# Performance work log

Hardware: AMD Instinct MI355X
Metric: run time of the kernel (lower is better)

The kernel has to match this reference:

```python
import jax, jax.numpy as jnp
import numpy as np

B, S, D = 2, 2048, 2048
H = 16
HD = D // H  # 128


def setup_inputs() -> dict:
    key = jax.random.key(0)
    ks = jax.random.split(key, 9)
    s = 1.0 / np.sqrt(D)
    return {
        "hidden_states": jax.random.normal(ks[0], (B, S, D), dtype=jnp.float32),
        "Wq": jax.random.normal(ks[1], (D, D), dtype=jnp.float32) * s,
        "bq": jnp.zeros((D,), dtype=jnp.float32),
        "Wk": jax.random.normal(ks[2], (D, D), dtype=jnp.float32) * s,
        "bk": jnp.zeros((D,), dtype=jnp.float32),
        "Wv": jax.random.normal(ks[3], (D, D), dtype=jnp.float32) * s,
        "bv": jnp.zeros((D,), dtype=jnp.float32),
        "Wo": jax.random.normal(ks[4], (D, D), dtype=jnp.float32) * s,
        "bo": jnp.zeros((D,), dtype=jnp.float32),
    }


def reference(hidden_states, Wq, bq, Wk, bk, Wv, bv, Wo, bo):
    x = hidden_states
    # linear projections (torch Linear: x @ W.T + b)
    q = x @ Wq.T + bq
    k = x @ Wk.T + bk
    v = x @ Wv.T + bv
    # [B, S, H, HD] -> [B, H, S, HD]
    q = q.reshape(B, S, H, HD).transpose(0, 2, 1, 3)
    k = k.reshape(B, S, H, HD).transpose(0, 2, 1, 3)
    v = v.reshape(B, S, H, HD).transpose(0, 2, 1, 3)
    q = q / jnp.sqrt(jnp.float32(HD))
    # scores [B, H, S, S]
    scores = jnp.einsum("bhqd,bhkd->bhqk", q, k)
    causal = jnp.triu(jnp.full((S, S), -jnp.inf, dtype=scores.dtype), k=1)
    scores = scores + causal
    attn = jax.nn.softmax(scores, axis=-1)
    out = jnp.einsum("bhqk,bhkd->bhqd", attn, v)
    out = out.transpose(0, 2, 1, 3).reshape(B, S, D)
    return out @ Wo.T + bo
```

## Files before the change

### kernel.cpp

```cpp
#include <hip/hip_runtime.h>
#include <stdint.h>

#define S_LEN 2048
#define DMODEL 2048
#define NHEAD 16
#define HDIM 128

typedef __attribute__((ext_vector_type(8))) short short8;
typedef __attribute__((ext_vector_type(4))) float floatx4;

__device__ __forceinline__ unsigned short f2b(float f) {
  union { float f; unsigned u; } v; v.f = f;
  unsigned r = v.u + 0x7FFFu + ((v.u >> 16) & 1u);
  return (unsigned short)(r >> 16);
}

__device__ __forceinline__ void load_lds16(const unsigned short* g, unsigned short* l) {
  __builtin_amdgcn_global_load_lds((const __attribute__((address_space(1))) void*)g,
                                   (__attribute__((address_space(3))) void*)l, 16, 0, 0);
}

__global__ __launch_bounds__(256) void cvt_all(const float* __restrict__ x,
                                               const float* __restrict__ Wq, const float* __restrict__ Wk,
                                               const float* __restrict__ Wv, const float* __restrict__ Wo,
                                               unsigned short* __restrict__ xb,
                                               unsigned short* __restrict__ Wqb, unsigned short* __restrict__ Wkb,
                                               unsigned short* __restrict__ Wvb, unsigned short* __restrict__ Wob) {
  const size_t idx = (size_t)blockIdx.x * 256 + threadIdx.x;
  const int y = blockIdx.y;
  const float4* s; ushort4* d;
  if (y == 0)      { s = (const float4*)x;               d = (ushort4*)xb; }
  else if (y == 1) { s = (const float4*)x + (1u << 20);  d = (ushort4*)xb + (1u << 20); }
  else if (y == 2) { s = (const float4*)Wq;              d = (ushort4*)Wqb; }
  else if (y == 3) { s = (const float4*)Wk;              d = (ushort4*)Wkb; }
  else if (y == 4) { s = (const float4*)Wv;              d = (ushort4*)Wvb; }
  else             { s = (const float4*)Wo;              d = (ushort4*)Wob; }
  float4 f = s[idx];
  ushort4 o;
  o.x = f2b(f.x); o.y = f2b(f.y); o.z = f2b(f.z); o.w = f2b(f.w);
  d[idx] = o;
}

template <int MODE>
__global__ __launch_bounds__(256)
void gemm_bt(const unsigned short* __restrict__ A, const unsigned short* __restrict__ Bw,
             const float* __restrict__ bias, void* __restrict__ Cout,
             int M, int N, int K, float scale) {
  __shared__ unsigned short As[128 * 64];
  __shared__ unsigned short Bs[128 * 64];
  const int t = threadIdx.x;
  const int lane = t & 63, wave = t >> 6;
  const int quad = lane >> 4, lc = lane & 15;
  const int wm = wave >> 1, wn = wave & 1;
  const int m0 = blockIdx.y * 128, n0 = blockIdx.x * 128;

  const int srow = lane >> 3;
  const int skoff = ((lane & 7) ^ srow) * 8;
  const unsigned short* Ag[4];
  const unsigned short* Bg[4];
  unsigned short* Al[4];
  unsigned short* Bl[4];
#pragma unroll
  for (int i = 0; i < 4; i++) {
    int c = wave * 4 + i;
    Ag[i] = A + (size_t)(m0 + c * 8 + srow) * K + skoff;
    Bg[i] = Bw + (size_t)(n0 + c * 8 + srow) * K + skoff;
    Al[i] = &As[c * 512 + lane * 8];
    Bl[i] = &Bs[c * 512 + lane * 8];
  }

  int koff[2];
#pragma unroll
  for (int ks = 0; ks < 2; ks++) koff[ks] = ((ks * 4 + quad) ^ (lc & 7)) * 8;

  floatx4 acc[4][4] = {};

  for (int kt = 0; kt < K; kt += 64) {
    if (kt) __syncthreads();
#pragma unroll
    for (int i = 0; i < 4; i++) {
      load_lds16(Ag[i] + kt, Al[i]);
      load_lds16(Bg[i] + kt, Bl[i]);
    }
    __syncthreads();
#pragma unroll
    for (int ks = 0; ks < 2; ks++) {
      short8 av[4], bv[4];
#pragma unroll
      for (int mt = 0; mt < 4; mt++)
        av[mt] = *(const short8*)&As[(wm * 64 + mt * 16 + lc) * 64 + koff[ks]];
#pragma unroll
      for (int nt = 0; nt < 4; nt++)
        bv[nt] = *(const short8*)&Bs[(wn * 64 + nt * 16 + lc) * 64 + koff[ks]];
#pragma unroll
      for (int mt = 0; mt < 4; mt++)
#pragma unroll
        for (int nt = 0; nt < 4; nt++)
          acc[mt][nt] = __builtin_amdgcn_mfma_f32_16x16x32_bf16(av[mt], bv[nt], acc[mt][nt], 0, 0, 0);
    }
  }

#pragma unroll
  for (int nt = 0; nt < 4; nt++) {
    const int col = n0 + wn * 64 + nt * 16 + lc;
    const float bcol = bias[col];
#pragma unroll
    for (int mt = 0; mt < 4; mt++) {
      const int row0 = m0 + wm * 64 + mt * 16 + quad * 4;
      if (MODE == 1) {
        ushort4 o;
        o.x = f2b((acc[mt][nt][0] + bcol) * scale);
        o.y = f2b((acc[mt][nt][1] + bcol) * scale);
        o.z = f2b((acc[mt][nt][2] + bcol) * scale);
        o.w = f2b((acc[mt][nt][3] + bcol) * scale);
        int b = row0 >> 11;
        int s = row0 & (S_LEN - 1);
        *(ushort4*)&((unsigned short*)Cout)[((size_t)(b * DMODEL + col)) * S_LEN + s] = o;
      } else {
#pragma unroll
        for (int r = 0; r < 4; r++) {
          float v = (acc[mt][nt][r] + bcol) * scale;
          if (MODE == 2)
            ((float*)Cout)[(size_t)(row0 + r) * N + col] = v;
          else
            ((unsigned short*)Cout)[(size_t)(row0 + r) * N + col] = f2b(v);
        }
      }
    }
  }
}

__global__ __launch_bounds__(256, 2)
void attn_fwd(const unsigned short* __restrict__ Qg, const unsigned short* __restrict__ Kg,
              const unsigned short* __restrict__ Vtg, unsigned short* __restrict__ Og) {
  __shared__ unsigned short Ks[2][64 * 128];
  __shared__ unsigned short Vs[128 * 64];
  __shared__ unsigned short Ps[128 * 64];

  const int t = threadIdx.x;
  const int lane = t & 63, w = t >> 6;
  const int quad = lane >> 4, lc = lane & 15;
  const int y = blockIdx.y;
  const int tile = (y < 16) ? (int)blockIdx.x : 15 - (int)blockIdx.x;
  const int b = y >> 4, h = y & 15;
  const size_t qkbase = (size_t)b * S_LEN * DMODEL + h * HDIM;
  const size_t vtbase = ((size_t)(b * DMODEL + h * HDIM)) * S_LEN;
  const int q0 = tile * 128;
  const int wrow = q0 + w * 32;

  short8 aq[2][4];
#pragma unroll
  for (int pm = 0; pm < 2; pm++)
#pragma unroll
    for (int ks = 0; ks < 4; ks++)
      aq[pm][ks] = *(const short8*)&Qg[qkbase + (size_t)(wrow + pm * 16 + lc) * DMODEL + ks * 32 + quad * 8];

  const unsigned short* kga[4];
  const unsigned short* vga[4];
  int kloff[4], vloff[4];
#pragma unroll
  for (int i = 0; i < 4; i++) {
    int c = w * 4 + i;
    int krow = 4 * c + (lane >> 4);
    kga[i] = Kg + qkbase + (size_t)krow * DMODEL + ((lane & 15) ^ (krow & 15)) * 8;
    kloff[i] = c * 512 + lane * 8;
    int vrow = 8 * c + (lane >> 3);
    vga[i] = Vtg + vtbase + (size_t)vrow * S_LEN + ((lane & 7) ^ (vrow & 7)) * 8;
    vloff[i] = c * 512 + lane * 8;
  }

  floatx4 oacc[2][8] = {};
  float m_run[2][4], l_run[2][4];
#pragma unroll
  for (int pm = 0; pm < 2; pm++)
#pragma unroll
    for (int r = 0; r < 4; r++) { m_run[pm][r] = -1e30f; l_run[pm][r] = 0.f; }

  const int kiters = 2 * tile + 2;

#pragma unroll
  for (int i = 0; i < 4; i++) load_lds16(kga[i], &Ks[0][kloff[i]]);

  for (int kb = 0; kb < kiters; kb++) {
    const int k0 = kb * 64;
    const int cur = kb & 1;
    __syncthreads();

#pragma unroll
    for (int i = 0; i < 4; i++) load_lds16(vga[i] + k0, &Vs[vloff[i]]);
    {
      const size_t knext = (size_t)((kb + 1 < kiters) ? k0 + 64 : k0) * DMODEL;
#pragma unroll
      for (int i = 0; i < 4; i++) load_lds16(kga[i] + knext, &Ks[cur ^ 1][kloff[i]]);
    }

    const bool hasw = (k0 <= wrow + 31);
    floatx4 sacc[2][4];
    float alpha[2][4];
    if (hasw) {
#pragma unroll
      for (int pm = 0; pm < 2; pm++)
#pragma unroll
        for (int nt = 0; nt < 4; nt++) sacc[pm][nt] = (floatx4){0.f, 0.f, 0.f, 0.f};
#pragma unroll
      for (int ks = 0; ks < 4; ks++) {
        short8 bk[4];
#pragma unroll
        for (int nt = 0; nt < 4; nt++) {
          int n = nt * 16 + lc;
          bk[nt] = *(const short8*)&Ks[cur][n * 128 + (((ks * 4 + quad) ^ (n & 15)) * 8)];
        }
#pragma unroll
        for (int pm = 0; pm < 2; pm++)
#pragma unroll
          for (int nt = 0; nt < 4; nt++)
            sacc[pm][nt] = __builtin_amdgcn_mfma_f32_16x16x32_bf16(aq[pm][ks], bk[nt], sacc[pm][nt], 0, 0, 0);
      }

      float mx[2][4];
#pragma unroll
      for (int pm = 0; pm < 2; pm++)
#pragma unroll
        for (int r = 0; r < 4; r++) mx[pm][r] = -1e30f;
      if (k0 + 63 > wrow) {
#pragma unroll
        for (int pm = 0; pm < 2; pm++)
#pragma unroll
          for (int nt = 0; nt < 4; nt++) {
            int col = k0 + nt * 16 + lc;
#pragma unroll
            for (int r = 0; r < 4; r++) {
              if (col > wrow + pm * 16 + quad * 4 + r) sacc[pm][nt][r] = -1e30f;
              mx[pm][r] = fmaxf(mx[pm][r], sacc[pm][nt][r]);
            }
          }
      } else {
#pragma unroll
        for (int pm = 0; pm < 2; pm++)
#pragma unroll
          for (int nt = 0; nt < 4; nt++)
#pragma unroll
            for (int r = 0; r < 4; r++) mx[pm][r] = fmaxf(mx[pm][r], sacc[pm][nt][r]);
      }
#pragma unroll
      for (int off = 1; off < 16; off <<= 1)
#pragma unroll
        for (int pm = 0; pm < 2; pm++)
#pragma unroll
          for (int r = 0; r < 4; r++) mx[pm][r] = fmaxf(mx[pm][r], __shfl_xor(mx[pm][r], off));

#pragma unroll
      for (int pm = 0; pm < 2; pm++)
#pragma unroll
        for (int r = 0; r < 4; r++) {
          float mnew = fmaxf(m_run[pm][r], mx[pm][r]);
          alpha[pm][r] = __builtin_amdgcn_exp2f(m_run[pm][r] - mnew);
          m_run[pm][r] = mnew;
          l_run[pm][r] *= alpha[pm][r];
        }
#pragma unroll
      for (int pm = 0; pm < 2; pm++)
#pragma unroll
        for (int nt = 0; nt < 4; nt++) {
#pragma unroll
          for (int r = 0; r < 4; r++) {
            float p = __builtin_amdgcn_exp2f(sacc[pm][nt][r] - m_run[pm][r]);
            l_run[pm][r] += p;
            int row = w * 32 + pm * 16 + quad * 4 + r;
            int sw = (((nt * 2 + (lc >> 3)) ^ (row & 7)) * 8) + (lc & 7);
            Ps[row * 64 + sw] = f2b(p);
          }
        }
    }

    asm volatile("s_waitcnt vmcnt(4)\n\ts_barrier" ::: "memory");

    if (hasw) {
#pragma unroll
      for (int pm = 0; pm < 2; pm++)
#pragma unroll
        for (int nt8 = 0; nt8 < 8; nt8++)
#pragma unroll
          for (int r = 0; r < 4; r++) oacc[pm][nt8][r] *= alpha[pm][r];

#pragma unroll
      for (int ks = 0; ks < 2; ks++) {
        short8 ap[2];
#pragma unroll
        for (int pm = 0; pm < 2; pm++) {
          int m = w * 32 + pm * 16 + lc;
          ap[pm] = *(const short8*)&Ps[m * 64 + (((ks * 4 + quad) ^ (m & 7)) * 8)];
        }
#pragma unroll
        for (int nt8 = 0; nt8 < 8; nt8++) {
          int n = nt8 * 16 + lc;
          short8 bv = *(const short8*)&Vs[n * 64 + (((ks * 4 + quad) ^ (n & 7)) * 8)];
#pragma unroll
          for (int pm = 0; pm < 2; pm++)
            oacc[pm][nt8] = __builtin_amdgcn_mfma_f32_16x16x32_bf16(ap[pm], bv, oacc[pm][nt8], 0, 0, 0);
        }
      }
    }
  }

#pragma unroll
  for (int off = 1; off < 16; off <<= 1)
#pragma unroll
    for (int pm = 0; pm < 2; pm++)
#pragma unroll
      for (int r = 0; r < 4; r++) l_run[pm][r] += __shfl_xor(l_run[pm][r], off);
#pragma unroll
  for (int pm = 0; pm < 2; pm++)
#pragma unroll
    for (int r = 0; r < 4; r++) {
      float inv = 1.f / l_run[pm][r];
      size_t obase = ((size_t)(b * S_LEN + wrow + pm * 16 + quad * 4 + r)) * DMODEL + h * HDIM;
#pragma unroll
      for (int nt8 = 0; nt8 < 8; nt8++)
        Og[obase + nt8 * 16 + lc] = f2b(oacc[pm][nt8][r] * inv);
    }
}

extern "C" void kernel_launch(void* const* d_in, const int* in_sizes, int n_in,
                              void* d_out, int out_size, void* d_ws, size_t ws_size,
                              hipStream_t stream) {
  const float* x  = (const float*)d_in[0];
  const float* Wq = (const float*)d_in[1];
  const float* bq = (const float*)d_in[2];
  const float* Wk = (const float*)d_in[3];
  const float* bk = (const float*)d_in[4];
  const float* Wv = (const float*)d_in[5];
  const float* bv = (const float*)d_in[6];
  const float* Wo = (const float*)d_in[7];
  const float* bo = (const float*)d_in[8];

  const int M = 2 * S_LEN;
  const int N = DMODEL, K = DMODEL;

  char* w = (char*)d_ws;
  unsigned short* xb  = (unsigned short*)(w);
  unsigned short* Wqb = (unsigned short*)(w + (size_t)16 * (1 << 20));
  unsigned short* Wkb = (unsigned short*)(w + (size_t)24 * (1 << 20));
  unsigned short* Wvb = (unsigned short*)(w + (size_t)32 * (1 << 20));
  unsigned short* Wob = (unsigned short*)(w + (size_t)40 * (1 << 20));
  unsigned short* Qb  = (unsigned short*)(w + (size_t)48 * (1 << 20));
  unsigned short* Kb  = (unsigned short*)(w + (size_t)64 * (1 << 20));
  unsigned short* Vtb = (unsigned short*)(w + (size_t)80 * (1 << 20));
  unsigned short* Ob  = (unsigned short*)(w + (size_t)96 * (1 << 20));

  cvt_all<<<dim3(4096, 6), 256, 0, stream>>>(x, Wq, Wk, Wv, Wo, xb, Wqb, Wkb, Wvb, Wob);

  dim3 gg(N / 128, M / 128);
  const float qscale = 0.08838834764831843f * 1.4426950408889634f;
  gemm_bt<0><<<gg, 256, 0, stream>>>(xb, Wqb, bq, Qb, M, N, K, qscale);
  gemm_bt<0><<<gg, 256, 0, stream>>>(xb, Wkb, bk, Kb, M, N, K, 1.f);
  gemm_bt<1><<<gg, 256, 0, stream>>>(xb, Wvb, bv, Vtb, M, N, K, 1.f);

  attn_fwd<<<dim3(16, 32), 256, 0, stream>>>(Qb, Kb, Vtb, Ob);

  gemm_bt<2><<<gg, 256, 0, stream>>>(Ob, Wob, bo, d_out, M, N, K, 1.f);
}
```

Measured before the change: 396.5 us.

## Compute transposed S and O tiles so each lane owns a query row

Swaps MFMA operand order so score and output accumulators are transposed, with each lane holding one query row. The row max and row sum then need only two cross-lane shuffles instead of four per element group, and running max/sum state shrinks to two scalars per lane. P is written to LDS as packed 4-element vectors in a padded (stride 72) layout instead of scalar swizzled stores, and output is stored as ushort4. The padded P buffer uses slightly more LDS.

```diff
diff --git a/kernel.cpp b/kernel.cpp
--- a/kernel.cpp
+++ b/kernel.cpp
@@ -135,7 +135,7 @@
               const unsigned short* __restrict__ Vtg, unsigned short* __restrict__ Og) {
   __shared__ unsigned short Ks[2][64 * 128];
   __shared__ unsigned short Vs[128 * 64];
-  __shared__ unsigned short Ps[128 * 64];
+  __shared__ unsigned short Ps[128 * 72];
 
   const int t = threadIdx.x;
   const int lane = t & 63, w = t >> 6;
@@ -169,12 +169,8 @@
     vloff[i] = c * 512 + lane * 8;
   }
 
-  floatx4 oacc[2][8] = {};
-  float m_run[2][4], l_run[2][4];
-#pragma unroll
-  for (int pm = 0; pm < 2; pm++)
-#pragma unroll
-    for (int r = 0; r < 4; r++) { m_run[pm][r] = -1e30f; l_run[pm][r] = 0.f; }
+  floatx4 oaccT[8][2] = {};
+  float m_run[2] = {-1e30f, -1e30f}, l_run[2] = {0.f, 0.f};
 
   const int kiters = 2 * tile + 2;
 
@@ -195,130 +191,121 @@
     }
 
     const bool hasw = (k0 <= wrow + 31);
-    floatx4 sacc[2][4];
-    float alpha[2][4];
+    float alpha[2];
     if (hasw) {
-#pragma unroll
-      for (int pm = 0; pm < 2; pm++)
-#pragma unroll
-        for (int nt = 0; nt < 4; nt++) sacc[pm][nt] = (floatx4){0.f, 0.f, 0.f, 0.f};
+      floatx4 st[4][2];
+#pragma unroll
+      for (int mt = 0; mt < 4; mt++)
+#pragma unroll
+        for (int pm = 0; pm < 2; pm++) st[mt][pm] = (floatx4){0.f, 0.f, 0.f, 0.f};
 #pragma unroll
       for (int ks = 0; ks < 4; ks++) {
-        short8 bk[4];
-#pragma unroll
-        for (int nt = 0; nt < 4; nt++) {
-          int n = nt * 16 + lc;
-          bk[nt] = *(const short8*)&Ks[cur][n * 128 + (((ks * 4 + quad) ^ (n & 15)) * 8)];
-        }
-#pragma unroll
-        for (int pm = 0; pm < 2; pm++)
-#pragma unroll
-          for (int nt = 0; nt < 4; nt++)
-            sacc[pm][nt] = __builtin_amdgcn_mfma_f32_16x16x32_bf16(aq[pm][ks], bk[nt], sacc[pm][nt], 0, 0, 0);
-      }
-
-      float mx[2][4];
-#pragma unroll
-      for (int pm = 0; pm < 2; pm++)
-#pragma unroll
-        for (int r = 0; r < 4; r++) mx[pm][r] = -1e30f;
+        short8 kf[4];
+#pragma unroll
+        for (int mt = 0; mt < 4; mt++) {
+          int n = mt * 16 + lc;
+          kf[mt] = *(const short8*)&Ks[cur][n * 128 + (((ks * 4 + quad) ^ (n & 15)) * 8)];
+        }
+#pragma unroll
+        for (int mt = 0; mt < 4; mt++)
+#pragma unroll
+          for (int pm = 0; pm < 2; pm++)
+            st[mt][pm] = __builtin_amdgcn_mfma_f32_16x16x32_bf16(kf[mt], aq[pm][ks], st[mt][pm], 0, 0, 0);
+      }
+
+      float mx[2] = {-1e30f, -1e30f};
       if (k0 + 63 > wrow) {
 #pragma unroll
-        for (int pm = 0; pm < 2; pm++)
-#pragma unroll
-          for (int nt = 0; nt < 4; nt++) {
-            int col = k0 + nt * 16 + lc;
+        for (int pm = 0; pm < 2; pm++) {
+          const int qq = wrow + pm * 16 + lc;
+#pragma unroll
+          for (int mt = 0; mt < 4; mt++) {
+            const int key = k0 + mt * 16 + quad * 4;
 #pragma unroll
             for (int r = 0; r < 4; r++) {
-              if (col > wrow + pm * 16 + quad * 4 + r) sacc[pm][nt][r] = -1e30f;
-              mx[pm][r] = fmaxf(mx[pm][r], sacc[pm][nt][r]);
+              if (key + r > qq) st[mt][pm][r] = -1e30f;
+              mx[pm] = fmaxf(mx[pm], st[mt][pm][r]);
             }
           }
+        }
       } else {
 #pragma unroll
         for (int pm = 0; pm < 2; pm++)
 #pragma unroll
-          for (int nt = 0; nt < 4; nt++)
-#pragma unroll
-            for (int r = 0; r < 4; r++) mx[pm][r] = fmaxf(mx[pm][r], sacc[pm][nt][r]);
-      }
-#pragma unroll
-      for (int off = 1; off < 16; off <<= 1)
+          for (int mt = 0; mt < 4; mt++)
+#pragma unroll
+            for (int r = 0; r < 4; r++) mx[pm] = fmaxf(mx[pm], st[mt][pm][r]);
+      }
+#pragma unroll
+      for (int pm = 0; pm < 2; pm++) {
+        mx[pm] = fmaxf(mx[pm], __shfl_xor(mx[pm], 16));
+        mx[pm] = fmaxf(mx[pm], __shfl_xor(mx[pm], 32));
+        float mnew = fmaxf(m_run[pm], mx[pm]);
+        alpha[pm] = __builtin_amdgcn_exp2f(m_run[pm] - mnew);
+        m_run[pm] = mnew;
+        l_run[pm] *= alpha[pm];
+      }
+
+#pragma unroll
+      for (int pm = 0; pm < 2; pm++)
+#pragma unroll
+        for (int mt = 0; mt < 4; mt++) {
+          float p0 = __builtin_amdgcn_exp2f(st[mt][pm][0] - m_run[pm]);
+          float p1 = __builtin_amdgcn_exp2f(st[mt][pm][1] - m_run[pm]);
+          float p2 = __builtin_amdgcn_exp2f(st[mt][pm][2] - m_run[pm]);
+          float p3 = __builtin_amdgcn_exp2f(st[mt][pm][3] - m_run[pm]);
+          l_run[pm] += (p0 + p1) + (p2 + p3);
+          ushort4 o;
+          o.x = f2b(p0); o.y = f2b(p1); o.z = f2b(p2); o.w = f2b(p3);
+          *(ushort4*)&Ps[(w * 32 + pm * 16 + lc) * 72 + mt * 16 + quad * 4] = o;
+        }
+    }
+
+    asm volatile("s_waitcnt vmcnt(4)\n\ts_barrier" ::: "memory");
+
+    if (hasw) {
+#pragma unroll
+      for (int mt8 = 0; mt8 < 8; mt8++)
+#pragma unroll
+        for (int pm = 0; pm < 2; pm++) {
+          oaccT[mt8][pm][0] *= alpha[pm]; oaccT[mt8][pm][1] *= alpha[pm];
+          oaccT[mt8][pm][2] *= alpha[pm]; oaccT[mt8][pm][3] *= alpha[pm];
+        }
+
+#pragma unroll
+      for (int ks = 0; ks < 2; ks++) {
+        short8 pf[2];
 #pragma unroll
         for (int pm = 0; pm < 2; pm++)
-#pragma unroll
-          for (int r = 0; r < 4; r++) mx[pm][r] = fmaxf(mx[pm][r], __shfl_xor(mx[pm][r], off));
-
-#pragma unroll
-      for (int pm = 0; pm < 2; pm++)
-#pragma unroll
-        for (int r = 0; r < 4; r++) {
-          float mnew = fmaxf(m_run[pm][r], mx[pm][r]);
-          alpha[pm][r] = __builtin_amdgcn_exp2f(m_run[pm][r] - mnew);
-          m_run[pm][r] = mnew;
-          l_run[pm][r] *= alpha[pm][r];
-        }
-#pragma unroll
-      for (int pm = 0; pm < 2; pm++)
-#pragma unroll
-        for (int nt = 0; nt < 4; nt++) {
-#pragma unroll
-          for (int r = 0; r < 4; r++) {
-            float p = __builtin_amdgcn_exp2f(sacc[pm][nt][r] - m_run[pm][r]);
-            l_run[pm][r] += p;
-            int row = w * 32 + pm * 16 + quad * 4 + r;
-            int sw = (((nt * 2 + (lc >> 3)) ^ (row & 7)) * 8) + (lc & 7);
-            Ps[row * 64 + sw] = f2b(p);
-          }
-        }
-    }
-
-    asm volatile("s_waitcnt vmcnt(4)\n\ts_barrier" ::: "memory");
-
-    if (hasw) {
-#pragma unroll
-      for (int pm = 0; pm < 2; pm++)
-#pragma unroll
-        for (int nt8 = 0; nt8 < 8; nt8++)
-#pragma unroll
-          for (int r = 0; r < 4; r++) oacc[pm][nt8][r] *= alpha[pm][r];
-
-#pragma unroll
-      for (int ks = 0; ks < 2; ks++) {
-        short8 ap[2];
-#pragma unroll
-        for (int pm = 0; pm < 2; pm++) {
-          int m = w * 32 + pm * 16 + lc;
-          ap[pm] = *(const short8*)&Ps[m * 64 + (((ks * 4 + quad) ^ (m & 7)) * 8)];
-        }
-#pragma unroll
-        for (int nt8 = 0; nt8 < 8; nt8++) {
-          int n = nt8 * 16 + lc;
-          short8 bv = *(const short8*)&Vs[n * 64 + (((ks * 4 + quad) ^ (n & 7)) * 8)];
+          pf[pm] = *(const short8*)&Ps[(w * 32 + pm * 16 + lc) * 72 + ks * 32 + quad * 8];
+#pragma unroll
+        for (int mt8 = 0; mt8 < 8; mt8++) {
+          int n = mt8 * 16 + lc;
+          short8 vf = *(const short8*)&Vs[n * 64 + (((ks * 4 + quad) ^ (n & 7)) * 8)];
 #pragma unroll
           for (int pm = 0; pm < 2; pm++)
-            oacc[pm][nt8] = __builtin_amdgcn_mfma_f32_16x16x32_bf16(ap[pm], bv, oacc[pm][nt8], 0, 0, 0);
-        }
-      }
-    }
-  }
-
-#pragma unroll
-  for (int off = 1; off < 16; off <<= 1)
-#pragma unroll
-    for (int pm = 0; pm < 2; pm++)
-#pragma unroll
-      for (int r = 0; r < 4; r++) l_run[pm][r] += __shfl_xor(l_run[pm][r], off);
-#pragma unroll
-  for (int pm = 0; pm < 2; pm++)
-#pragma unroll
-    for (int r = 0; r < 4; r++) {
-      float inv = 1.f / l_run[pm][r];
-      size_t obase = ((size_t)(b * S_LEN + wrow + pm * 16 + quad * 4 + r)) * DMODEL + h * HDIM;
-#pragma unroll
-      for (int nt8 = 0; nt8 < 8; nt8++)
-        Og[obase + nt8 * 16 + lc] = f2b(oacc[pm][nt8][r] * inv);
-    }
+            oaccT[mt8][pm] = __builtin_amdgcn_mfma_f32_16x16x32_bf16(vf, pf[pm], oaccT[mt8][pm], 0, 0, 0);
+        }
+      }
+    }
+  }
+
+#pragma unroll
+  for (int pm = 0; pm < 2; pm++) {
+    l_run[pm] += __shfl_xor(l_run[pm], 16);
+    l_run[pm] += __shfl_xor(l_run[pm], 32);
+    float inv = 1.f / l_run[pm];
+    size_t obase = ((size_t)(b * S_LEN + wrow + pm * 16 + lc)) * DMODEL + h * HDIM;
+#pragma unroll
+    for (int mt8 = 0; mt8 < 8; mt8++) {
+      ushort4 o;
+      o.x = f2b(oaccT[mt8][pm][0] * inv);
+      o.y = f2b(oaccT[mt8][pm][1] * inv);
+      o.z = f2b(oaccT[mt8][pm][2] * inv);
+      o.w = f2b(oaccT[mt8][pm][3] * inv);
+      *(ushort4*)&Og[obase + mt8 * 16 + quad * 4] = o;
+    }
+  }
 }
 
 extern "C" void kernel_launch(void* const* d_in, const int* in_sizes, int n_in,
```

Result: faster. 379.4 us (-4.3%).
